# Kernel tuning notes

Measured on AMD Instinct MI355X. Metric: run time of the kernel, lower is better.

The kernel has to match this reference:

```python
import jax, jax.numpy as jnp
import numpy as np

M, N, D = 16384, 128, 2048  # actions, question tokens, ExpSet.dim


def setup_inputs() -> dict:
    key = jax.random.key(0)
    ks = jax.random.split(key, 6)
    s1 = 1.0 / np.sqrt(2 * D)  # torch Linear default init bounds
    s2 = 1.0 / np.sqrt(D)
    return {
        "action_embedding": jax.random.normal(ks[0], (M, D), jnp.float32),
        "question_t": jax.random.normal(ks[1], (N, D), jnp.float32),
        "history_t": jax.random.normal(ks[2], (D,), jnp.float32),
        "W1": jax.random.uniform(ks[3], (D, 2 * D), jnp.float32, -s1, s1),
        "b1": jnp.zeros((D,), jnp.float32),
        "W2": jax.random.uniform(ks[4], (D, D), jnp.float32, -s2, s2),
        "b2": jnp.zeros((D,), jnp.float32),
    }


def reference(action_embedding, question_t, history_t, W1, b1, W2, b2):
    # Attention: each action (query) attends over the n question tokens.
    # Equivalent to expand->attend->sum in the torch code, but without
    # materializing the [m, n, d] expanded tensor.
    scores = action_embedding @ question_t.T              # [M, N]
    attn = jax.nn.softmax(scores, axis=1)                 # softmax over tokens
    question = attn @ question_t                          # [M, D] (attended + summed)

    # Perceptron(2d -> d -> d) on cat([history, question])
    hist = jnp.broadcast_to(history_t, (action_embedding.shape[0], history_t.shape[0]))
    qh = jnp.concatenate([hist, question], axis=1)        # [M, 2D]
    h = jax.nn.relu(qh @ W1.T + b1)                       # [M, D]
    qwh = h @ W2.T + b2                                   # [M, D]

    # Elementwise dot with action embeddings, softmax over actions.
    semantic_scores = jnp.sum(qwh * action_embedding, axis=1)  # [M]
    return jax.nn.softmax(semantic_scores, axis=0)
```

## Files before the change

kernel.cpp:

```cpp
#include <hip/hip_runtime.h>
#include <hip/hip_bf16.h>


typedef _Float16 f16;
typedef __attribute__((ext_vector_type(8))) _Float16 half8;
typedef __attribute__((ext_vector_type(4))) _Float16 half4_t;
typedef __attribute__((ext_vector_type(4))) float f32x4;

#define GLL(gp, lp)                                                              \
  __builtin_amdgcn_global_load_lds(                                              \
      (const __attribute__((address_space(1))) void*)(gp),                       \
      (__attribute__((address_space(3))) void*)(lp), 16, 0, 0)

#define WAITN(n)                                                                 \
  do {                                                                           \
    asm volatile("s_waitcnt vmcnt(" #n ")" ::: "memory");                        \
    __builtin_amdgcn_sched_barrier(0);                                           \
  } while (0)

#define MFMA16(a, b, c) __builtin_amdgcn_mfma_f32_16x16x32_f16(a, b, c, 0, 0, 0)

template <int NT, int LDA, int LDB>
__device__ __forceinline__ void kloop1(const f16* __restrict__ A,
                                       const f16* __restrict__ B,
                                       f16* __restrict__ SM,
                                       f32x4 (&acc)[4][4],
                                       int lane, int wv, int wm, int wn) {
  static_assert(NT >= 4, "depth-3 pipeline needs NT >= 4");
  const int f = lane & 15, kk = lane >> 4;
  const int cS = (lane & 7) ^ (lane >> 3);
  const int kkS = (cS & 3) * 8;
  const int rS = 2 * (lane >> 3) + (cS >> 2);
  const size_t offA0 = (size_t)(16 * (wv * 2 + 0) + rS) * LDA + kkS;
  const size_t offA1 = (size_t)(16 * (wv * 2 + 1) + rS) * LDA + kkS;
  const size_t offB0 = (size_t)(16 * (wv * 2 + 0) + rS) * LDB + kkS;
  const size_t offB1 = (size_t)(16 * (wv * 2 + 1) + rS) * LDB + kkS;
  const int Ld0 = (wv * 2 + 0) * 512, Ld1 = (wv * 2 + 1) * 512;

  int aoff[4], boff[4];
  #pragma unroll
  for (int mf = 0; mf < 4; ++mf) {
    const int R = wm + mf * 16 + f;
    const int c2 = (((R & 1) << 2) | kk) ^ ((R >> 1) & 7);
    aoff[mf] = (R >> 1) * 64 + c2 * 8;
  }
  #pragma unroll
  for (int nf = 0; nf < 4; ++nf) {
    const int R = wn + nf * 16 + f;
    const int c2 = (((R & 1) << 2) | kk) ^ ((R >> 1) & 7);
    boff[nf] = (R >> 1) * 64 + c2 * 8;
  }

  auto STAGE = [&](int set, int kt) {
    f16* base = SM + set * 8192;
    GLL(A + offA0 + kt, base + Ld0);
    GLL(A + offA1 + kt, base + Ld1);
    GLL(B + offB0 + kt, base + 4096 + Ld0);
    GLL(B + offB1 + kt, base + 4096 + Ld1);
  };
  auto COMPUTE = [&](int set) {
    const f16* p = SM + set * 8192;
    half8 a[4], b[4];
    #pragma unroll
    for (int mf = 0; mf < 4; ++mf) a[mf] = *(const half8*)&p[aoff[mf]];
    #pragma unroll
    for (int nf = 0; nf < 4; ++nf) b[nf] = *(const half8*)&p[4096 + boff[nf]];
    __builtin_amdgcn_s_setprio(1);
    #pragma unroll
    for (int mf = 0; mf < 4; ++mf)
      #pragma unroll
      for (int nf = 0; nf < 4; ++nf)
        acc[mf][nf] = MFMA16(a[mf], b[nf], acc[mf][nf]);
    __builtin_amdgcn_s_setprio(0);
  };

  STAGE(0, 0);
  STAGE(1, 32);
  STAGE(2, 64);
  #pragma unroll 1
  for (int t = 0; t < NT - 3; ++t) {
    STAGE((t + 3) & 3, (t + 3) * 32);
    WAITN(12);
    __builtin_amdgcn_s_barrier();
    COMPUTE(t & 3);
    __builtin_amdgcn_s_barrier();
  }
  WAITN(8);
  __builtin_amdgcn_s_barrier();
  COMPUTE((NT - 3) & 3);
  __builtin_amdgcn_s_barrier();
  WAITN(4);
  __builtin_amdgcn_s_barrier();
  COMPUTE((NT - 2) & 3);
  __builtin_amdgcn_s_barrier();
  WAITN(0);
  __builtin_amdgcn_s_barrier();
  COMPUTE((NT - 1) & 3);
  __builtin_amdgcn_s_barrier();
}


__global__ __launch_bounds__(256) void c_kernel(const float* __restrict__ W1,
                                                const float* __restrict__ b1,
                                                const float* __restrict__ hist,
                                                float* __restrict__ c) {
  const int wave = threadIdx.x >> 6, lane = threadIdx.x & 63;
  const int j = blockIdx.x * 4 + wave;
  const float* row = W1 + (size_t)j * 4096;
  float s = 0.f;
  #pragma unroll 2
  for (int kq = lane; kq < 512; kq += 64) {
    const float4 w = *(const float4*)&row[kq * 4];
    const float4 h = *(const float4*)&hist[kq * 4];
    s += w.x * h.x + w.y * h.y + w.z * h.z + w.w * h.w;
  }
  #pragma unroll
  for (int mask = 1; mask < 64; mask <<= 1) s += __shfl_xor(s, mask);
  if (lane == 0) c[j] = s + b1[j];
}

__device__ __forceinline__ half4_t f16hi4(const float4 v) {
  half4_t h;
  h.x = (f16)v.x; h.y = (f16)v.y; h.z = (f16)v.z; h.w = (f16)v.w;
  return h;
}

__global__ __launch_bounds__(256) void prep_AQ(const float* __restrict__ A,
                                               const float* __restrict__ Q,
                                               const float* __restrict__ b2,
                                               f16* __restrict__ Af,
                                               f16* __restrict__ Qf,
                                               float* __restrict__ ab2) {
  const int wv = threadIdx.x >> 6, lane = threadIdx.x & 63;
  if (blockIdx.x < 4096) {
    const size_t row = (size_t)blockIdx.x * 4 + wv;
    const float* ar = A + row * 2048;
    float dot = 0.f;
    #pragma unroll 2
    for (int c0 = 0; c0 < 2048; c0 += 256) {
      const int col = c0 + lane * 4;
      const float4 v = *(const float4*)&ar[col];
      const float4 bb = *(const float4*)&b2[col];
      dot += v.x * bb.x + v.y * bb.y + v.z * bb.z + v.w * bb.w;
      *(half4_t*)&Af[row * 2048 + col] = f16hi4(v);
    }
    #pragma unroll
    for (int mask = 1; mask < 64; mask <<= 1) dot += __shfl_xor(dot, mask);
    if (lane == 0) ab2[row] = dot;
  } else {
    const size_t row = (size_t)(blockIdx.x - 4096) * 4 + wv;
    const float* qr = Q + row * 2048;
    #pragma unroll 2
    for (int c0 = 0; c0 < 2048; c0 += 256) {
      const int col = c0 + lane * 4;
      const float4 v = *(const float4*)&qr[col];
      *(half4_t*)&Qf[row * 2048 + col] = f16hi4(v);
    }
  }
}

__global__ __launch_bounds__(256) void transpose_pack(const float* __restrict__ src,
                                                      f16* __restrict__ W2p) {
  __shared__ float T[64][65];
  const int c0 = blockIdx.x * 64, r0 = blockIdx.y * 64;
  const int t = threadIdx.x;
  {
    const int rl = t >> 4, cl = (t & 15) * 4;
    #pragma unroll
    for (int ii = 0; ii < 4; ++ii) {
      const float4 v = *(const float4*)&src[(size_t)(r0 + rl + ii * 16) * 2048 + c0 + cl];
      T[rl + ii * 16][cl + 0] = v.x; T[rl + ii * 16][cl + 1] = v.y;
      T[rl + ii * 16][cl + 2] = v.z; T[rl + ii * 16][cl + 3] = v.w;
    }
  }
  __syncthreads();
  const int cc = t >> 2, rr0 = (t & 3) * 16;
  f16 u[16];
  #pragma unroll
  for (int k = 0; k < 16; ++k) u[k] = (f16)T[rr0 + k][cc];
  const int j = c0 + cc;
  const int k0 = r0 + rr0;
  const int rb = j >> 4, f = j & 15;
  const int kb = k0 >> 5, kk0 = (k0 & 31) >> 3;
  f16* p0 = W2p + ((size_t)(rb * 64 + kb) * 64 + kk0 * 16 + f) * 8;
  f16* p1 = W2p + ((size_t)(rb * 64 + kb) * 64 + (kk0 + 1) * 16 + f) * 8;
  *(half4_t*)&p0[0] = *(half4_t*)&u[0];
  *(half4_t*)&p0[4] = *(half4_t*)&u[4];
  *(half4_t*)&p1[0] = *(half4_t*)&u[8];
  *(half4_t*)&p1[4] = *(half4_t*)&u[12];
}

template <int BM, int TM>
__global__ __launch_bounds__(256) void gemm_bt_sk(const float* __restrict__ A,
                                                  const float* __restrict__ B,
                                                  float* __restrict__ Cpart,
                                                  int Kslab, int lda, int ldb,
                                                  int ldc, int M) {
  constexpr int BN = 64, BK = 32;
  constexpr int ASTR = BM + 12, BSTR = BN + 4;
  __shared__ float As[BK][ASTR];
  __shared__ float Bs[BK][BSTR];
  const int tid = threadIdx.x;
  const int tx = tid & 15, ty = tid >> 4;
  const int m0 = ty * TM, n0 = tx * 4;
  const size_t bm = (size_t)blockIdx.x * BM, bn = (size_t)blockIdx.y * BN;
  const int kb = blockIdx.z * Kslab;
  const float* Ab = A + bm * lda;
  const float* Bb = B + bn * ldb;
  float acc[TM][4];
  #pragma unroll
  for (int i = 0; i < TM; ++i)
    #pragma unroll
    for (int j = 0; j < 4; ++j) acc[i][j] = 0.f;
  for (int kt = kb; kt < kb + Kslab; kt += BK) {
    #pragma unroll
    for (int it = 0; it < BM * BK / 4 / 256; ++it) {
      const int idx = it * 256 + tid;
      const int row = idx >> 3, kq = idx & 7;
      const float4 v = *(const float4*)&Ab[(size_t)row * lda + kt + kq * 4];
      As[kq * 4 + 0][row] = v.x; As[kq * 4 + 1][row] = v.y;
      As[kq * 4 + 2][row] = v.z; As[kq * 4 + 3][row] = v.w;
    }
    #pragma unroll
    for (int it = 0; it < BN * BK / 4 / 256; ++it) {
      const int idx = it * 256 + tid;
      const int row = idx >> 3, kq = idx & 7;
      const float4 v = *(const float4*)&Bb[(size_t)row * ldb + kt + kq * 4];
      Bs[kq * 4 + 0][row] = v.x; Bs[kq * 4 + 1][row] = v.y;
      Bs[kq * 4 + 2][row] = v.z; Bs[kq * 4 + 3][row] = v.w;
    }
    __syncthreads();
    #pragma unroll
    for (int k = 0; k < BK; ++k) {
      float av[TM];
      #pragma unroll
      for (int i = 0; i < TM; ++i) av[i] = As[k][m0 + i];
      const float4 b = *(const float4*)&Bs[k][n0];
      const float bv[4] = {b.x, b.y, b.z, b.w};
      #pragma unroll
      for (int i = 0; i < TM; ++i)
        #pragma unroll
        for (int j = 0; j < 4; ++j) acc[i][j] = fmaf(av[i], bv[j], acc[i][j]);
    }
    __syncthreads();
  }
  float* base = Cpart + (size_t)blockIdx.z * M * ldc;
  #pragma unroll
  for (int i = 0; i < TM; ++i) {
    float* crow = base + (bm + m0 + i) * (size_t)ldc + bn + n0;
    #pragma unroll
    for (int j = 0; j < 4; ++j) crow[j] = acc[i][j];
  }
}

__global__ __launch_bounds__(256) void qwt_combine(const float* __restrict__ part,
                                                   f16* __restrict__ QWt) {
  const size_t i = ((size_t)blockIdx.x * 256 + threadIdx.x) * 4;
  float4 s = make_float4(0.f, 0.f, 0.f, 0.f);
  #pragma unroll
  for (int z = 0; z < 8; ++z) {
    const float4 v = *(const float4*)&part[(size_t)z * 262144 + i];
    s.x += v.x; s.y += v.y; s.z += v.z; s.w += v.w;
  }
  *(half4_t*)&QWt[i] = f16hi4(s);
}

__global__ __launch_bounds__(256, 2) void s_attn_sk(const f16* __restrict__ Af,
                                                    const f16* __restrict__ Qf,
                                                    float* __restrict__ Sp) {
  __shared__ f16 SM[32768];
  const int tid = threadIdx.x, lane = tid & 63, wv = tid >> 6;
  const int wm = (wv >> 1) * 64, wn = (wv & 1) * 64;
  const int f = lane & 15, kk = lane >> 4;
  const size_t bm = (size_t)(blockIdx.x >> 1) * 128;
  const int kz = blockIdx.x & 1;

  f32x4 acc[4][4];
  #pragma unroll
  for (int mf = 0; mf < 4; ++mf)
    #pragma unroll
    for (int nf = 0; nf < 4; ++nf) acc[mf][nf] = 0.f;

  kloop1<32, 2048, 2048>(Af + bm * 2048 + kz * 1024, Qf + kz * 1024,
                         SM, acc, lane, wv, wm, wn);

  float* out = Sp + (size_t)kz * 16384 * 128;
  #pragma unroll
  for (int mf = 0; mf < 4; ++mf)
    #pragma unroll
    for (int r = 0; r < 4; ++r) {
      const size_t row = bm + wm + mf * 16 + kk * 4 + r;
      #pragma unroll
      for (int nf = 0; nf < 4; ++nf)
        out[row * 128 + wn + nf * 16 + f] = acc[mf][nf][r];
    }
}

__global__ __launch_bounds__(256) void softmax_at(const float* __restrict__ Sp,
                                                  f16* __restrict__ at) {
  const int tid = threadIdx.x;
  const int sub = tid & 7;
  const size_t row = (size_t)blockIdx.x * 32 + (tid >> 3);
  const float* p0 = Sp + row * 128 + sub * 16;
  const float* p1 = p0 + (size_t)16384 * 128;
  float v[16];
  #pragma unroll
  for (int q = 0; q < 4; ++q) {
    const float4 a = ((const float4*)p0)[q];
    const float4 b = ((const float4*)p1)[q];
    v[q * 4 + 0] = a.x + b.x; v[q * 4 + 1] = a.y + b.y;
    v[q * 4 + 2] = a.z + b.z; v[q * 4 + 3] = a.w + b.w;
  }
  float mx = v[0];
  #pragma unroll
  for (int e = 1; e < 16; ++e) mx = fmaxf(mx, v[e]);
  mx = fmaxf(mx, __shfl_xor(mx, 1));
  mx = fmaxf(mx, __shfl_xor(mx, 2));
  mx = fmaxf(mx, __shfl_xor(mx, 4));
  float sm = 0.f;
  #pragma unroll
  for (int e = 0; e < 16; ++e) { v[e] = __expf(v[e] - mx); sm += v[e]; }
  sm += __shfl_xor(sm, 1);
  sm += __shfl_xor(sm, 2);
  sm += __shfl_xor(sm, 4);
  const float inv = 1.0f / sm;
  f16* po = at + row * 128 + sub * 16;
  #pragma unroll
  for (int q = 0; q < 4; ++q) {
    half4_t h;
    h.x = (f16)(v[q * 4 + 0] * inv); h.y = (f16)(v[q * 4 + 1] * inv);
    h.z = (f16)(v[q * 4 + 2] * inv); h.w = (f16)(v[q * 4 + 3] * inv);
    *(half4_t*)&po[q * 4] = h;
  }
}

__global__ __launch_bounds__(256, 2) void h_kernel(const f16* __restrict__ at,
                                                   const f16* __restrict__ QWt,
                                                   const float* __restrict__ cvec,
                                                   f16* __restrict__ H) {
  __shared__ f16 SM[32768];
  const int tid = threadIdx.x, lane = tid & 63, wv = tid >> 6;
  const int wm = (wv >> 1) * 64, wn = (wv & 1) * 64;
  const int f = lane & 15, kk = lane >> 4;
  const size_t bm = (size_t)(blockIdx.x & 127) * 128;
  const size_t bn = (size_t)(blockIdx.x >> 7) * 128;

  f32x4 acc[4][4];
  #pragma unroll
  for (int mf = 0; mf < 4; ++mf)
    #pragma unroll
    for (int nf = 0; nf < 4; ++nf) acc[mf][nf] = 0.f;

  kloop1<4, 128, 128>(at + bm * 128, QWt + bn * 128, SM, acc, lane, wv, wm, wn);

  float ccv[4];
  #pragma unroll
  for (int nf = 0; nf < 4; ++nf) ccv[nf] = cvec[bn + wn + nf * 16 + f];

  __syncthreads();
  constexpr int STR = 136;
  f16* T = SM;
  #pragma unroll
  for (int mf = 0; mf < 4; ++mf)
    #pragma unroll
    for (int r = 0; r < 4; ++r) {
      const int row = wm + mf * 16 + kk * 4 + r;
      #pragma unroll
      for (int nf = 0; nf < 4; ++nf)
        T[row * STR + wn + nf * 16 + f] =
            (f16)fmaxf(acc[mf][nf][r] + ccv[nf], 0.f);
    }
  __syncthreads();
  #pragma unroll
  for (int it = 0; it < 8; ++it) {
    const int row = it * 16 + (tid >> 4);
    const int ch = tid & 15;
    const float4 vv = *(const float4*)&T[row * STR + ch * 8];
    *(float4*)&H[(bm + row) * 2048 + bn + ch * 8] = vv;
  }
}

__global__ __launch_bounds__(512, 1) void fused_g(
    const f16* __restrict__ Af, const f16* __restrict__ H,
    const f16* __restrict__ W2p, float* __restrict__ partial) {
  extern __shared__ f16 SM[];
  const int tid = threadIdx.x, lane = tid & 63, wv = tid >> 6;
  const int wm = (wv >> 1) * 64;
  const int wn = (wv & 1) * 128;
  const int f = lane & 15, kk = lane >> 4;
  const int lin = blockIdx.x;
  const int sid = (lin & 7) * 64 + (lin >> 3);
  const int bmI = sid & 63, bnI = sid >> 6;
  const size_t bm = (size_t)bmI * 256;
  const size_t bn = (size_t)bnI * 256;
  const f16* A = Af + bm * 2048;
  const int rbase = (int)(bn >> 4) + (wn >> 4);

  const int cS = (lane & 7) ^ (lane >> 3);
  const int kkS = (cS & 3) * 8;
  const int rS = 2 * (lane >> 3) + (cS >> 2);
  const size_t offA0 = (size_t)(16 * (wv * 2 + 0) + rS) * 2048 + kkS;
  const size_t offA1 = (size_t)(16 * (wv * 2 + 1) + rS) * 2048 + kkS;
  const int Ld0 = (wv * 2 + 0) * 512, Ld1 = (wv * 2 + 1) * 512;

  int aoff[4];
  #pragma unroll
  for (int mf = 0; mf < 4; ++mf) {
    const int R = wm + mf * 16 + f;
    const int c2 = (((R & 1) << 2) | kk) ^ ((R >> 1) & 7);
    aoff[mf] = (R >> 1) * 64 + c2 * 8;
  }

  f32x4 acc[4][8];
  #pragma unroll
  for (int mf = 0; mf < 4; ++mf)
    #pragma unroll
    for (int nf = 0; nf < 8; ++nf) acc[mf][nf] = 0.f;

  half8 bA[8], bB[8];

#define STAGE_A(set, kt)                                                         \
  do {                                                                           \
    f16* base_ = SM + (set) * 8192;                                              \
    GLL(A + offA0 + (kt), base_ + Ld0);                                          \
    GLL(A + offA1 + (kt), base_ + Ld1);                                          \
  } while (0)

#define BLOAD(dst, t)                                                            \
  do {                                                                           \
    _Pragma("unroll")                                                            \
    for (int nf = 0; nf < 8; ++nf)                                               \
      dst[nf] = *(const half8*)&W2p[((size_t)(rbase + nf) * 64 + (t)) * 512 +    \
                                    lane * 8];                                   \
  } while (0)

#define COMPUTE(set, b)                                                          \
  do {                                                                           \
    const f16* p_ = SM + (set) * 8192;                                           \
    half8 a_[4];                                                                 \
    _Pragma("unroll")                                                            \
    for (int mf = 0; mf < 4; ++mf) a_[mf] = *(const half8*)&p_[aoff[mf]];        \
    __builtin_amdgcn_s_setprio(1);                                               \
    _Pragma("unroll")                                                            \
    for (int mf = 0; mf < 4; ++mf)                                               \
      _Pragma("unroll")                                                          \
      for (int nf = 0; nf < 8; ++nf)                                             \
        acc[mf][nf] = MFMA16(a_[mf], b[nf], acc[mf][nf]);                        \
    __builtin_amdgcn_s_setprio(0);                                               \
  } while (0)

  BLOAD(bA, 0);
  STAGE_A(0, 0);
  STAGE_A(1, 32);
  #pragma unroll 1
  for (int t = 0; t < 62; t += 2) {
    BLOAD(bB, t + 1);
    STAGE_A((t + 2) & 3, (t + 2) * 32);
    WAITN(10);
    __builtin_amdgcn_s_barrier();
    COMPUTE(t & 3, bA);
    BLOAD(bA, t + 2);
    STAGE_A((t + 3) & 3, (t + 3) * 32);
    WAITN(10);
    __builtin_amdgcn_s_barrier();
    COMPUTE((t + 1) & 3, bB);
  }
  BLOAD(bB, 63);
  WAITN(8);
  __builtin_amdgcn_s_barrier();
  COMPUTE(2, bA);
  WAITN(0);
  __builtin_amdgcn_s_barrier();
  COMPUTE(3, bB);

#undef STAGE_A
#undef BLOAD
#undef COMPUTE

  #pragma unroll
  for (int mf = 0; mf < 4; ++mf)
    #pragma unroll
    for (int r = 0; r < 4; ++r) {
      const size_t hrow = (bm + wm + mf * 16 + kk * 4 + r) * 2048 + bn + wn + f;
      float s = 0.f;
      #pragma unroll
      for (int nf = 0; nf < 8; ++nf)
        s += (float)H[hrow + nf * 16] * acc[mf][nf][r];
      s += __shfl_xor(s, 1);
      s += __shfl_xor(s, 2);
      s += __shfl_xor(s, 4);
      s += __shfl_xor(s, 8);
      if (f == 0) {
        const size_t slab = (size_t)(bnI * 2 + (wv & 1)) * 16384;
        partial[slab + bm + wm + mf * 16 + kk * 4 + r] = s;
      }
    }
}


__global__ __launch_bounds__(256) void k_sem(const float* __restrict__ partial,
                                             const float* __restrict__ ab2,
                                             float* __restrict__ semantic,
                                             float* __restrict__ bstats) {
  const int m = blockIdx.x * 256 + threadIdx.x;
  float s = ab2[m];
  #pragma unroll
  for (int nb = 0; nb < 16; ++nb) s += partial[(size_t)nb * 16384 + m];
  semantic[m] = s;
  float mx = s;
  #pragma unroll
  for (int mask = 1; mask < 64; mask <<= 1) mx = fmaxf(mx, __shfl_xor(mx, mask));
  __shared__ float wmax[4], wsum[4];
  const int wave = threadIdx.x >> 6, lane = threadIdx.x & 63;
  if (lane == 0) wmax[wave] = mx;
  __syncthreads();
  const float bmax = fmaxf(fmaxf(wmax[0], wmax[1]), fmaxf(wmax[2], wmax[3]));
  float e = expf(s - bmax);
  #pragma unroll
  for (int mask = 1; mask < 64; mask <<= 1) e += __shfl_xor(e, mask);
  if (lane == 0) wsum[wave] = e;
  __syncthreads();
  if (threadIdx.x == 0) {
    bstats[blockIdx.x * 2] = bmax;
    bstats[blockIdx.x * 2 + 1] = wsum[0] + wsum[1] + wsum[2] + wsum[3];
  }
}

__global__ __launch_bounds__(256) void k_out(const float* __restrict__ semantic,
                                             const float* __restrict__ bstats,
                                             float* __restrict__ out) {
  __shared__ float g0s, g1s;
  const int tid = threadIdx.x;
  if (tid < 64) {
    const float bm = bstats[tid * 2], bs = bstats[tid * 2 + 1];
    float gm = bm;
    #pragma unroll
    for (int mask = 1; mask < 64; mask <<= 1) gm = fmaxf(gm, __shfl_xor(gm, mask));
    float gs = bs * expf(bm - gm);
    #pragma unroll
    for (int mask = 1; mask < 64; mask <<= 1) gs += __shfl_xor(gs, mask);
    if (tid == 0) { g0s = gm; g1s = gs; }
  }
  __syncthreads();
  const int m = blockIdx.x * 256 + tid;
  out[m] = expf(semantic[m] - g0s) / g1s;
}


extern "C" void kernel_launch(void* const* d_in, const int* in_sizes, int n_in,
                              void* d_out, int out_size, void* d_ws, size_t ws_size,
                              hipStream_t stream) {
  (void)in_sizes; (void)n_in; (void)out_size; (void)ws_size;
  const float* A    = (const float*)d_in[0];
  const float* Q    = (const float*)d_in[1];
  const float* hist = (const float*)d_in[2];
  const float* W1   = (const float*)d_in[3];
  const float* b1   = (const float*)d_in[4];
  const float* W2   = (const float*)d_in[5];
  const float* b2   = (const float*)d_in[6];
  float* out = (float*)d_out;

  char* ws = (char*)d_ws;
  f16* Af      = (f16*)ws;   ws += (size_t)16384 * 2048 * 2;
  f16* Hbuf    = (f16*)ws;   ws += (size_t)16384 * 2048 * 2;
  f16* W2p     = (f16*)ws;   ws += (size_t)2048 * 2048 * 2;
  f16* Qf      = (f16*)ws;   ws += (size_t)128 * 2048 * 2;
  f16* QWt     = (f16*)ws;   ws += (size_t)2048 * 128 * 2;
  f16* at      = (f16*)ws;   ws += (size_t)16384 * 128 * 2;
  float* qwt_part = (float*)ws; ws += (size_t)8 * 2048 * 128 * 4;
  float* Sp    = (float*)ws; ws += (size_t)2 * 16384 * 128 * 4;
  float* c_vec = (float*)ws; ws += 2048 * 4;
  float* ab2   = (float*)ws; ws += 16384 * 4;
  float* partial  = (float*)ws; ws += (size_t)16 * 16384 * 4;
  float* semantic = (float*)ws; ws += 16384 * 4;
  float* bstats   = (float*)ws; ws += 128 * 4;

  hipFuncSetAttribute((const void*)fused_g,
                      hipFuncAttributeMaxDynamicSharedMemorySize, 65536);

  c_kernel<<<512, 256, 0, stream>>>(W1, b1, hist, c_vec);
  gemm_bt_sk<32, 2><<<dim3(64, 2, 8), 256, 0, stream>>>(W1 + 2048, Q, qwt_part,
                                                        256, 4096, 2048, 128, 2048);
  qwt_combine<<<256, 256, 0, stream>>>(qwt_part, QWt);
  transpose_pack<<<dim3(32, 32), 256, 0, stream>>>(W2, W2p);
  prep_AQ<<<4128, 256, 0, stream>>>(A, Q, b2, Af, Qf, ab2);
  s_attn_sk<<<256, 256, 0, stream>>>(Af, Qf, Sp);
  softmax_at<<<512, 256, 0, stream>>>(Sp, at);
  h_kernel<<<2048, 256, 0, stream>>>(at, QWt, c_vec, Hbuf);
  fused_g<<<512, 512, 65536, stream>>>(Af, Hbuf, W2p, partial);
  k_sem<<<64, 256, 0, stream>>>(partial, ab2, semantic, bstats);
  k_out<<<64, 256, 0, stream>>>(semantic, bstats, out);
}
```

Baseline: 289.8 us.

## Drop B-register double buffering in fused_g loop and enlarge dynamic LDS

Replaces the manually unrolled two-step loop, which prefetched W2 fragments into alternating register sets, with a single-step loop that loads B fragments right before use. It waits with vmcnt(12) and stages A two tiles ahead. The dynamic shared memory request grows from 64KB to 96KB, though only 4 sets of 8192 halves (64KB) are indexed. Freeing the extra B register set may reduce register pressure, at the risk of exposing global-load latency for B. The larger LDS request may also lower occupancy.

```diff
diff --git a/kernel.cpp b/kernel.cpp
--- a/kernel.cpp
+++ b/kernel.cpp
@@ -417,8 +417,6 @@
     #pragma unroll
     for (int nf = 0; nf < 8; ++nf) acc[mf][nf] = 0.f;
 
-  half8 bA[8], bB[8];
-
 #define STAGE_A(set, kt)                                                         \
   do {                                                                           \
     f16* base_ = SM + (set) * 8192;                                              \
@@ -426,56 +424,33 @@
     GLL(A + offA1 + (kt), base_ + Ld1);                                          \
   } while (0)
 
-#define BLOAD(dst, t)                                                            \
-  do {                                                                           \
-    _Pragma("unroll")                                                            \
-    for (int nf = 0; nf < 8; ++nf)                                               \
-      dst[nf] = *(const half8*)&W2p[((size_t)(rbase + nf) * 64 + (t)) * 512 +    \
-                                    lane * 8];                                   \
-  } while (0)
-
-#define COMPUTE(set, b)                                                          \
-  do {                                                                           \
-    const f16* p_ = SM + (set) * 8192;                                           \
-    half8 a_[4];                                                                 \
-    _Pragma("unroll")                                                            \
-    for (int mf = 0; mf < 4; ++mf) a_[mf] = *(const half8*)&p_[aoff[mf]];        \
-    __builtin_amdgcn_s_setprio(1);                                               \
-    _Pragma("unroll")                                                            \
-    for (int mf = 0; mf < 4; ++mf)                                               \
-      _Pragma("unroll")                                                          \
-      for (int nf = 0; nf < 8; ++nf)                                             \
-        acc[mf][nf] = MFMA16(a_[mf], b[nf], acc[mf][nf]);                        \
-    __builtin_amdgcn_s_setprio(0);                                               \
-  } while (0)
-
-  BLOAD(bA, 0);
   STAGE_A(0, 0);
   STAGE_A(1, 32);
   #pragma unroll 1
-  for (int t = 0; t < 62; t += 2) {
-    BLOAD(bB, t + 1);
-    STAGE_A((t + 2) & 3, (t + 2) * 32);
-    WAITN(10);
+  for (int t = 0; t < 64; ++t) {
+    half8 b[8];
+    #pragma unroll
+    for (int nf = 0; nf < 8; ++nf)
+      b[nf] = *(const half8*)&W2p[((size_t)(rbase + nf) * 64 + t) * 512 +
+                                  lane * 8];
+    if (t < 62) STAGE_A((t + 2) & 3, (t + 2) * 32);
+    WAITN(12);
     __builtin_amdgcn_s_barrier();
-    COMPUTE(t & 3, bA);
-    BLOAD(bA, t + 2);
-    STAGE_A((t + 3) & 3, (t + 3) * 32);
-    WAITN(10);
-    __builtin_amdgcn_s_barrier();
-    COMPUTE((t + 1) & 3, bB);
-  }
-  BLOAD(bB, 63);
-  WAITN(8);
-  __builtin_amdgcn_s_barrier();
-  COMPUTE(2, bA);
-  WAITN(0);
-  __builtin_amdgcn_s_barrier();
-  COMPUTE(3, bB);
-
+    {
+      const f16* p = SM + (t & 3) * 8192;
+      half8 a[4];
+      #pragma unroll
+      for (int mf = 0; mf < 4; ++mf) a[mf] = *(const half8*)&p[aoff[mf]];
+      __builtin_amdgcn_s_setprio(1);
+      #pragma unroll
+      for (int mf = 0; mf < 4; ++mf)
+        #pragma unroll
+        for (int nf = 0; nf < 8; ++nf)
+          acc[mf][nf] = MFMA16(a[mf], b[nf], acc[mf][nf]);
+      __builtin_amdgcn_s_setprio(0);
+    }
+  }
 #undef STAGE_A
-#undef BLOAD
-#undef COMPUTE
 
   #pragma unroll
   for (int mf = 0; mf < 4; ++mf)
@@ -576,7 +551,7 @@
   float* bstats   = (float*)ws; ws += 128 * 4;
 
   hipFuncSetAttribute((const void*)fused_g,
-                      hipFuncAttributeMaxDynamicSharedMemorySize, 65536);
+                      hipFuncAttributeMaxDynamicSharedMemorySize, 98304);
 
   c_kernel<<<512, 256, 0, stream>>>(W1, b1, hist, c_vec);
   gemm_bt_sk<32, 2><<<dim3(64, 2, 8), 256, 0, stream>>>(W1 + 2048, Q, qwt_part,
@@ -587,7 +562,7 @@
   s_attn_sk<<<256, 256, 0, stream>>>(Af, Qf, Sp);
   softmax_at<<<512, 256, 0, stream>>>(Sp, at);
   h_kernel<<<2048, 256, 0, stream>>>(at, QWt, c_vec, Hbuf);
-  fused_g<<<512, 512, 65536, stream>>>(Af, Hbuf, W2p, partial);
+  fused_g<<<512, 512, 98304, stream>>>(Af, Hbuf, W2p, partial);
   k_sem<<<64, 256, 0, stream>>>(partial, ab2, semantic, bstats);
   k_out<<<64, 256, 0, stream>>>(semantic, bstats, out);
 }
```

After: 269.7 us. -6.9%, faster.
